# Performance work log

Hardware: AMD Instinct MI355X
Metric: run time of the kernel (lower is better)

The kernel has to match this reference:

```python
import jax, jax.numpy as jnp
import numpy as np

E, N = 400000, 50000
D = 128          # efeat_dim = src_dim = dst_dim = output_dim
H = 512          # hidden_dim
CAT = 3 * D      # concat of [efeat, src, dst]
LN_EPS = 1e-5


def setup_inputs() -> dict:
    key = jax.random.key(0)
    ks = jax.random.split(key, 12)
    scale = 0.02
    return {
        "efeat": jax.random.normal(ks[0], (E, D), jnp.float32),
        "src_feat": jax.random.normal(ks[1], (N, D), jnp.float32),
        "dst_feat": jax.random.normal(ks[2], (N, D), jnp.float32),
        "src_idx": jax.random.randint(ks[3], (E,), 0, N),
        "dst_idx": jax.random.randint(ks[4], (E,), 0, N),
        # MLP params: Linear(CAT,H) -> SiLU -> Linear(H,H) -> SiLU -> Linear(H,D) -> LayerNorm(D)
        "W1": jax.random.normal(ks[5], (CAT, H), jnp.float32) * scale,
        "b1": jnp.zeros((H,), jnp.float32),
        "W2": jax.random.normal(ks[6], (H, H), jnp.float32) * scale,
        "b2": jnp.zeros((H,), jnp.float32),
        "W3": jax.random.normal(ks[7], (H, D), jnp.float32) * scale,
        "b3": jnp.zeros((D,), jnp.float32),
        "gamma": jnp.ones((D,), jnp.float32),
        "beta": jnp.zeros((D,), jnp.float32),
    }


def _layer_norm(y, gamma, beta):
    mu = jnp.mean(y, axis=-1, keepdims=True)
    var = jnp.mean(jnp.square(y - mu), axis=-1, keepdims=True)
    return (y - mu) * jax.lax.rsqrt(var + LN_EPS) * gamma + beta


def reference(efeat, src_feat, dst_feat, src_idx, dst_idx,
              W1, b1, W2, b2, W3, b3, gamma, beta):
    # concat_efeat: per-edge gather of src/dst node feats + concat with edge feats
    cat = jnp.concatenate([efeat, src_feat[src_idx], dst_feat[dst_idx]], axis=1)  # [E, 3D]
    h = jax.nn.silu(cat @ W1 + b1)   # [E, H]
    h = jax.nn.silu(h @ W2 + b2)     # [E, H]
    y = h @ W3 + b3                  # [E, D]
    return _layer_norm(y, gamma, beta)
```

## Files before the change

kernel.cpp:

```cpp
#include <hip/hip_runtime.h>
#include <hip/hip_bf16.h>
#include <cstdint>
#include <cstddef>

typedef __attribute__((ext_vector_type(4))) float f32x4;
typedef __attribute__((ext_vector_type(8))) short s16x8;
typedef __attribute__((ext_vector_type(4))) unsigned int u32x4;

#define E_ 400000
#define D_ 128
#define H_ 512
#define CAT_ 384
#define BM 64
#define NBLK 6250
#define SCRATCH 65536
#define LDS_TOTAL (65536 + 1024)

__device__ __forceinline__ unsigned cvtpk(float lo, float hi) {
  unsigned r;
  asm("v_cvt_pk_bf16_f32 %0, %1, %2" : "=v"(r) : "v"(lo), "v"(hi));
  return r;
}
__device__ __forceinline__ float silu_f(float x) {
  return x * __builtin_amdgcn_rcpf(1.0f + __expf(-x));
}

#define HS(row, byteoff) (smem + (row) * 1024 + ((byteoff) ^ (((row) & 7) << 4)))

__global__ __launch_bounds__(512, 4)
void edge_mlp_fused(const float* __restrict__ efeat,
                    const float* __restrict__ src_feat,
                    const float* __restrict__ dst_feat,
                    const int* __restrict__ src_idx,
                    const int* __restrict__ dst_idx,
                    const unsigned short* __restrict__ P1,
                    const unsigned short* __restrict__ P2,
                    const unsigned short* __restrict__ P3,
                    const float* __restrict__ b1,
                    const float* __restrict__ b2,
                    const float* __restrict__ b3,
                    const float* __restrict__ gamma,
                    const float* __restrict__ beta,
                    float* __restrict__ out) {
  extern __shared__ char smem[];
  const int tid = threadIdx.x;
  const int lane = tid & 63;
  const int wave = tid >> 6;
  const int lr = lane & 15;
  const int kc = lane >> 4;
  const int g4 = kc * 4;
  const size_t e0 = (size_t)blockIdx.x * BM;
  const int rot = ((blockIdx.x >> 8) & 1) << 3;

  const unsigned short* w1base = P1 + (size_t)kc * 4096 + wave * 512 + lr * 8;
  const unsigned short* w2base = P2 + (size_t)kc * 4096 + wave * 512 + lr * 8;

  const int grow = tid >> 3, gq = tid & 7;
  const size_t ee = e0 + grow;

#define LOAD4(dst, base) { const float* s0_ = (base) + gq * 8; \
  dst[0] = *(const f32x4*)s0_;        dst[1] = *(const f32x4*)(s0_ + 4); \
  dst[2] = *(const f32x4*)(s0_ + 64); dst[3] = *(const f32x4*)(s0_ + 68); }

#define STASH(v, scol) { \
  u32x4 r0_, r1_; \
  r0_.x = cvtpk(v[0][0], v[0][1]); r0_.y = cvtpk(v[0][2], v[0][3]); \
  r0_.z = cvtpk(v[1][0], v[1][1]); r0_.w = cvtpk(v[1][2], v[1][3]); \
  r1_.x = cvtpk(v[2][0], v[2][1]); r1_.y = cvtpk(v[2][2], v[2][3]); \
  r1_.z = cvtpk(v[3][0], v[3][1]); r1_.w = cvtpk(v[3][2], v[3][3]); \
  *(u32x4*)HS(grow, ((scol) + gq * 8) * 2) = r0_; \
  *(u32x4*)HS(grow, ((scol) + 64 + gq * 8) * 2) = r1_; }

  {
    f32x4 acc[4][4];
    #pragma unroll
    for (int eg = 0; eg < 4; ++eg)
      #pragma unroll
      for (int j = 0; j < 4; ++j) acc[eg][j] = (f32x4){0.f, 0.f, 0.f, 0.f};

    const float* psrc = src_feat + (size_t)src_idx[ee] * D_;
    const float* pdst = dst_feat + (size_t)dst_idx[ee] * D_;

    f32x4 gx[4], gs[4];
    LOAD4(gx, efeat + ee * D_);
    LOAD4(gs, psrc);
    STASH(gx, 0);

    asm volatile("s_waitcnt lgkmcnt(0)" ::: "memory");
    __builtin_amdgcn_s_barrier();
    asm volatile("" ::: "memory");

    auto g1tier = [&](int P0) {
      const unsigned short* wp = w1base + (size_t)P0 * 16384;
      #pragma unroll 1
      for (int pp = 0; pp < 4; ++pp) {
        s16x8 w[4];
        #pragma unroll
        for (int j = 0; j < 4; ++j)
          w[j] = *(const s16x8*)(wp + j * 128);
        const int p = P0 + pp;
        #pragma unroll
        for (int eg = 0; eg < 4; ++eg) {
          const s16x8 bf = *(const s16x8*)HS(eg * 16 + lr, p * 64 + kc * 16);
          #pragma unroll
          for (int j = 0; j < 4; ++j)
            acc[eg][j] = __builtin_amdgcn_mfma_f32_16x16x32_bf16(w[j], bf, acc[eg][j], 0, 0, 0);
        }
        wp += 16384;
      }
    };

    g1tier(0);
    STASH(gs, 128);
    LOAD4(gx, pdst);
    asm volatile("s_waitcnt lgkmcnt(0)" ::: "memory");
    __builtin_amdgcn_s_barrier();
    asm volatile("" ::: "memory");

    g1tier(4);
    STASH(gx, 256);
    asm volatile("s_waitcnt lgkmcnt(0)" ::: "memory");
    __builtin_amdgcn_s_barrier();
    asm volatile("" ::: "memory");

    g1tier(8);

    __builtin_amdgcn_s_barrier();
    asm volatile("" ::: "memory");

    #pragma unroll
    for (int j = 0; j < 4; ++j) {
      const int col0 = (wave * 4 + j) * 16 + g4;
      const f32x4 bv = *(const f32x4*)(b1 + col0);
      #pragma unroll
      for (int eg = 0; eg < 4; ++eg) {
        uint2 o_;
        o_.x = cvtpk(silu_f(acc[eg][j][0] + bv[0]), silu_f(acc[eg][j][1] + bv[1]));
        o_.y = cvtpk(silu_f(acc[eg][j][2] + bv[2]), silu_f(acc[eg][j][3] + bv[3]));
        *(uint2*)HS(eg * 16 + lr, col0 * 2) = o_;
      }
    }
  }
  asm volatile("s_waitcnt lgkmcnt(0)" ::: "memory");
  __builtin_amdgcn_s_barrier();
  asm volatile("" ::: "memory");

  {
    f32x4 acc[4][4];
    #pragma unroll
    for (int eg = 0; eg < 4; ++eg)
      #pragma unroll
      for (int j = 0; j < 4; ++j) acc[eg][j] = (f32x4){0.f, 0.f, 0.f, 0.f};

    #pragma unroll 2
    for (int pp = 0; pp < 16; ++pp) {
      const int p = (pp + rot) & 15;
      s16x8 w[4];
      #pragma unroll
      for (int j = 0; j < 4; ++j)
        w[j] = *(const s16x8*)(w2base + (size_t)p * 16384 + j * 128);
      #pragma unroll
      for (int eg = 0; eg < 4; ++eg) {
        const s16x8 bf = *(const s16x8*)HS(eg * 16 + lr, p * 64 + kc * 16);
        #pragma unroll
        for (int j = 0; j < 4; ++j)
          acc[eg][j] = __builtin_amdgcn_mfma_f32_16x16x32_bf16(w[j], bf, acc[eg][j], 0, 0, 0);
      }
    }

    __builtin_amdgcn_s_barrier();
    asm volatile("" ::: "memory");

    #pragma unroll
    for (int j = 0; j < 4; ++j) {
      const int col0 = (wave * 4 + j) * 16 + g4;
      const f32x4 bv = *(const f32x4*)(b2 + col0);
      #pragma unroll
      for (int eg = 0; eg < 4; ++eg) {
        uint2 o_;
        o_.x = cvtpk(silu_f(acc[eg][j][0] + bv[0]), silu_f(acc[eg][j][1] + bv[1]));
        o_.y = cvtpk(silu_f(acc[eg][j][2] + bv[2]), silu_f(acc[eg][j][3] + bv[3]));
        *(uint2*)HS(eg * 16 + lr, col0 * 2) = o_;
      }
    }
  }
  asm volatile("s_waitcnt lgkmcnt(0)" ::: "memory");
  __builtin_amdgcn_s_barrier();
  asm volatile("" ::: "memory");

  {
    const int eg3 = wave >> 1;
    const int half = wave & 1;
    const int edge = eg3 * 16 + lr;

    f32x4 acc[4];
    #pragma unroll
    for (int j = 0; j < 4; ++j) acc[j] = (f32x4){0.f, 0.f, 0.f, 0.f};

    const unsigned short* w3b = P3 + (size_t)kc * 1024 + half * 512 + lr * 8;

    #pragma unroll 2
    for (int pp = 0; pp < 16; ++pp) {
      const int p = (pp + rot) & 15;
      s16x8 w[4];
      #pragma unroll
      for (int j = 0; j < 4; ++j)
        w[j] = *(const s16x8*)(w3b + (size_t)p * 4096 + j * 128);
      const s16x8 bf = *(const s16x8*)HS(edge, p * 64 + kc * 16);
      #pragma unroll
      for (int j = 0; j < 4; ++j)
        acc[j] = __builtin_amdgcn_mfma_f32_16x16x32_bf16(w[j], bf, acc[j], 0, 0, 0);
    }

    float sum = 0.f, ss = 0.f;
    #pragma unroll
    for (int j = 0; j < 4; ++j) {
      const f32x4 bv = *(const f32x4*)(b3 + half * 64 + j * 16 + g4);
      #pragma unroll
      for (int r = 0; r < 4; ++r) {
        acc[j][r] += bv[r];
        sum += acc[j][r];
        ss += acc[j][r] * acc[j][r];
      }
    }
    sum += __shfl_xor(sum, 16, 64); ss += __shfl_xor(ss, 16, 64);
    sum += __shfl_xor(sum, 32, 64); ss += __shfl_xor(ss, 32, 64);

    if (lane < 16) {
      float2 pw; pw.x = sum; pw.y = ss;
      *(float2*)(smem + SCRATCH + edge * 16 + half * 8) = pw;
    }
    asm volatile("s_waitcnt lgkmcnt(0)" ::: "memory");
    __builtin_amdgcn_s_barrier();
    asm volatile("" ::: "memory");

    const f32x4 pt = *(const f32x4*)(smem + SCRATCH + edge * 16);
    const float sumT = pt[0] + pt[2];
    const float ssT  = pt[1] + pt[3];
    const float mu = sumT * (1.0f / 128.0f);
    const float var = ssT * (1.0f / 128.0f) - mu * mu;
    const float rstd = rsqrtf(var + 1e-5f);

    float* orow = out + (e0 + edge) * D_ + half * 64;
    #pragma unroll
    for (int j = 0; j < 4; ++j) {
      const f32x4 gv  = *(const f32x4*)(gamma + half * 64 + j * 16 + g4);
      const f32x4 btv = *(const f32x4*)(beta  + half * 64 + j * 16 + g4);
      f32x4 o;
      #pragma unroll
      for (int r = 0; r < 4; ++r)
        o[r] = (acc[j][r] - mu) * rstd * gv[r] + btv[r];
      *(f32x4*)(orow + j * 16 + g4) = o;
    }
  }
#undef LOAD4
#undef STASH
}

__global__ void prep_pack(const float* __restrict__ W, unsigned short* __restrict__ P,
                          int K, int N) {
  const int t = blockIdx.x * blockDim.x + threadIdx.x;
  if (t >= N * (K >> 3)) return;
  const int n = t % N;
  const int k8 = t / N;
  const int k0 = k8 << 3;
  const int p = k0 >> 5, kc = (k0 >> 3) & 3;
  s16x8 w;
  #pragma unroll
  for (int j = 0; j < 8; ++j) {
    union { float f; unsigned u; } t_; t_.f = W[(size_t)(k0 + j) * N + n];
    w[j] = (short)((t_.u + 0x8000u) >> 16);
  }
  *(s16x8*)(P + (size_t)p * N * 32 + (size_t)kc * N * 8 + (size_t)n * 8) = w;
}

extern "C" void kernel_launch(void* const* d_in, const int* in_sizes, int n_in,
                              void* d_out, int out_size, void* d_ws, size_t ws_size,
                              hipStream_t stream) {
  const float* efeat    = (const float*)d_in[0];
  const float* src_feat = (const float*)d_in[1];
  const float* dst_feat = (const float*)d_in[2];
  const int*   src_idx  = (const int*)d_in[3];
  const int*   dst_idx  = (const int*)d_in[4];
  const float* W1 = (const float*)d_in[5];
  const float* b1 = (const float*)d_in[6];
  const float* W2 = (const float*)d_in[7];
  const float* b2 = (const float*)d_in[8];
  const float* W3 = (const float*)d_in[9];
  const float* b3 = (const float*)d_in[10];
  const float* gamma = (const float*)d_in[11];
  const float* beta  = (const float*)d_in[12];

  unsigned short* P1 = (unsigned short*)d_ws;
  unsigned short* P2 = P1 + 196608;
  unsigned short* P3 = P2 + 262144;

  (void)hipFuncSetAttribute((const void*)edge_mlp_fused,
                            hipFuncAttributeMaxDynamicSharedMemorySize, LDS_TOTAL);

  prep_pack<<<(512 * 48 + 255) / 256, 256, 0, stream>>>(W1, P1, CAT_, H_);
  prep_pack<<<(512 * 64 + 255) / 256, 256, 0, stream>>>(W2, P2, H_, H_);
  prep_pack<<<(128 * 64 + 255) / 256, 256, 0, stream>>>(W3, P3, H_, D_);

  edge_mlp_fused<<<NBLK, 512, LDS_TOTAL, stream>>>(
      efeat, src_feat, dst_feat, src_idx, dst_idx,
      P1, P2, P3, b1, b2, b3, gamma, beta, (float*)d_out);
}
```

Before: 531.6 us.

## Double block to 1024 threads, halve per-wave columns, gather inputs upfront

Each block now runs 16 waves over the same 64 edges, so every wave owns 32 hidden columns instead of 64 and half as many accumulators. The staged overlap of gathering src/dst rows with the first GEMM is replaced by one gather of all three feature sources before the first GEMM. The aim is more waves in flight to hide memory latency and lighter register pressure per wave. The cost is that the gather no longer overlaps with compute, and the 1024-thread blocks with about 66KB LDS each may limit how many blocks fit per CU.

After: 543.4 us. 1.02x slower.

```diff
diff --git a/kernel.cpp b/kernel.cpp
--- a/kernel.cpp
+++ b/kernel.cpp
@@ -14,7 +14,7 @@
 #define BM 64
 #define NBLK 6250
 #define SCRATCH 65536
-#define LDS_TOTAL (65536 + 1024)
+#define LDS_TOTAL (65536 + 2048)
 
 __device__ __forceinline__ unsigned cvtpk(float lo, float hi) {
   unsigned r;
@@ -27,7 +27,7 @@
 
 #define HS(row, byteoff) (smem + (row) * 1024 + ((byteoff) ^ (((row) & 7) << 4)))
 
-__global__ __launch_bounds__(512, 4)
+__global__ __launch_bounds__(1024, 8)
 void edge_mlp_fused(const float* __restrict__ efeat,
                     const float* __restrict__ src_feat,
                     const float* __restrict__ dst_feat,
@@ -52,85 +52,59 @@
   const size_t e0 = (size_t)blockIdx.x * BM;
   const int rot = ((blockIdx.x >> 8) & 1) << 3;
 
-  const unsigned short* w1base = P1 + (size_t)kc * 4096 + wave * 512 + lr * 8;
-  const unsigned short* w2base = P2 + (size_t)kc * 4096 + wave * 512 + lr * 8;
-
-  const int grow = tid >> 3, gq = tid & 7;
-  const size_t ee = e0 + grow;
-
-#define LOAD4(dst, base) { const float* s0_ = (base) + gq * 8; \
-  dst[0] = *(const f32x4*)s0_;        dst[1] = *(const f32x4*)(s0_ + 4); \
-  dst[2] = *(const f32x4*)(s0_ + 64); dst[3] = *(const f32x4*)(s0_ + 68); }
-
-#define STASH(v, scol) { \
-  u32x4 r0_, r1_; \
-  r0_.x = cvtpk(v[0][0], v[0][1]); r0_.y = cvtpk(v[0][2], v[0][3]); \
-  r0_.z = cvtpk(v[1][0], v[1][1]); r0_.w = cvtpk(v[1][2], v[1][3]); \
-  r1_.x = cvtpk(v[2][0], v[2][1]); r1_.y = cvtpk(v[2][2], v[2][3]); \
-  r1_.z = cvtpk(v[3][0], v[3][1]); r1_.w = cvtpk(v[3][2], v[3][3]); \
-  *(u32x4*)HS(grow, ((scol) + gq * 8) * 2) = r0_; \
-  *(u32x4*)HS(grow, ((scol) + 64 + gq * 8) * 2) = r1_; }
-
-  {
-    f32x4 acc[4][4];
+  const unsigned short* w1base = P1 + (size_t)kc * 4096 + wave * 256 + lr * 8;
+  const unsigned short* w2base = P2 + (size_t)kc * 4096 + wave * 256 + lr * 8;
+
+  {
+    const int row = tid >> 4, q = tid & 15;
+    const size_t ee = e0 + row;
+    const float* bases[3];
+    bases[0] = efeat + ee * D_;
+    bases[1] = src_feat + (size_t)src_idx[ee] * D_;
+    bases[2] = dst_feat + (size_t)dst_idx[ee] * D_;
+    #pragma unroll
+    for (int s = 0; s < 3; ++s) {
+      const float* sp = bases[s] + q * 8;
+      const f32x4 v0 = *(const f32x4*)sp;
+      const f32x4 v1 = *(const f32x4*)(sp + 4);
+      u32x4 r_;
+      r_.x = cvtpk(v0[0], v0[1]); r_.y = cvtpk(v0[2], v0[3]);
+      r_.z = cvtpk(v1[0], v1[1]); r_.w = cvtpk(v1[2], v1[3]);
+      *(u32x4*)HS(row, (s * 128 + q * 8) * 2) = r_;
+    }
+  }
+  asm volatile("s_waitcnt lgkmcnt(0)" ::: "memory");
+  __builtin_amdgcn_s_barrier();
+  asm volatile("" ::: "memory");
+
+  {
+    f32x4 acc[4][2];
     #pragma unroll
     for (int eg = 0; eg < 4; ++eg)
       #pragma unroll
-      for (int j = 0; j < 4; ++j) acc[eg][j] = (f32x4){0.f, 0.f, 0.f, 0.f};
-
-    const float* psrc = src_feat + (size_t)src_idx[ee] * D_;
-    const float* pdst = dst_feat + (size_t)dst_idx[ee] * D_;
-
-    f32x4 gx[4], gs[4];
-    LOAD4(gx, efeat + ee * D_);
-    LOAD4(gs, psrc);
-    STASH(gx, 0);
-
-    asm volatile("s_waitcnt lgkmcnt(0)" ::: "memory");
+      for (int j = 0; j < 2; ++j) acc[eg][j] = (f32x4){0.f, 0.f, 0.f, 0.f};
+
+    #pragma unroll 2
+    for (int p = 0; p < 12; ++p) {
+      s16x8 w[2];
+      #pragma unroll
+      for (int j = 0; j < 2; ++j)
+        w[j] = *(const s16x8*)(w1base + (size_t)p * 16384 + j * 128);
+      #pragma unroll
+      for (int eg = 0; eg < 4; ++eg) {
+        const s16x8 bf = *(const s16x8*)HS(eg * 16 + lr, p * 64 + kc * 16);
+        #pragma unroll
+        for (int j = 0; j < 2; ++j)
+          acc[eg][j] = __builtin_amdgcn_mfma_f32_16x16x32_bf16(w[j], bf, acc[eg][j], 0, 0, 0);
+      }
+    }
+
     __builtin_amdgcn_s_barrier();
     asm volatile("" ::: "memory");
 
-    auto g1tier = [&](int P0) {
-      const unsigned short* wp = w1base + (size_t)P0 * 16384;
-      #pragma unroll 1
-      for (int pp = 0; pp < 4; ++pp) {
-        s16x8 w[4];
-        #pragma unroll
-        for (int j = 0; j < 4; ++j)
-          w[j] = *(const s16x8*)(wp + j * 128);
-        const int p = P0 + pp;
-        #pragma unroll
-        for (int eg = 0; eg < 4; ++eg) {
-          const s16x8 bf = *(const s16x8*)HS(eg * 16 + lr, p * 64 + kc * 16);
-          #pragma unroll
-          for (int j = 0; j < 4; ++j)
-            acc[eg][j] = __builtin_amdgcn_mfma_f32_16x16x32_bf16(w[j], bf, acc[eg][j], 0, 0, 0);
-        }
-        wp += 16384;
-      }
-    };
-
-    g1tier(0);
-    STASH(gs, 128);
-    LOAD4(gx, pdst);
-    asm volatile("s_waitcnt lgkmcnt(0)" ::: "memory");
-    __builtin_amdgcn_s_barrier();
-    asm volatile("" ::: "memory");
-
-    g1tier(4);
-    STASH(gx, 256);
-    asm volatile("s_waitcnt lgkmcnt(0)" ::: "memory");
-    __builtin_amdgcn_s_barrier();
-    asm volatile("" ::: "memory");
-
-    g1tier(8);
-
-    __builtin_amdgcn_s_barrier();
-    asm volatile("" ::: "memory");
-
-    #pragma unroll
-    for (int j = 0; j < 4; ++j) {
-      const int col0 = (wave * 4 + j) * 16 + g4;
+    #pragma unroll
+    for (int j = 0; j < 2; ++j) {
+      const int col0 = wave * 32 + j * 16 + g4;
       const f32x4 bv = *(const f32x4*)(b1 + col0);
       #pragma unroll
       for (int eg = 0; eg < 4; ++eg) {
@@ -146,24 +120,24 @@
   asm volatile("" ::: "memory");
 
   {
-    f32x4 acc[4][4];
+    f32x4 acc[4][2];
     #pragma unroll
     for (int eg = 0; eg < 4; ++eg)
       #pragma unroll
-      for (int j = 0; j < 4; ++j) acc[eg][j] = (f32x4){0.f, 0.f, 0.f, 0.f};
+      for (int j = 0; j < 2; ++j) acc[eg][j] = (f32x4){0.f, 0.f, 0.f, 0.f};
 
     #pragma unroll 2
     for (int pp = 0; pp < 16; ++pp) {
       const int p = (pp + rot) & 15;
-      s16x8 w[4];
-      #pragma unroll
-      for (int j = 0; j < 4; ++j)
+      s16x8 w[2];
+      #pragma unroll
+      for (int j = 0; j < 2; ++j)
         w[j] = *(const s16x8*)(w2base + (size_t)p * 16384 + j * 128);
       #pragma unroll
       for (int eg = 0; eg < 4; ++eg) {
         const s16x8 bf = *(const s16x8*)HS(eg * 16 + lr, p * 64 + kc * 16);
         #pragma unroll
-        for (int j = 0; j < 4; ++j)
+        for (int j = 0; j < 2; ++j)
           acc[eg][j] = __builtin_amdgcn_mfma_f32_16x16x32_bf16(w[j], bf, acc[eg][j], 0, 0, 0);
       }
     }
@@ -172,8 +146,8 @@
     asm volatile("" ::: "memory");
 
     #pragma unroll
-    for (int j = 0; j < 4; ++j) {
-      const int col0 = (wave * 4 + j) * 16 + g4;
+    for (int j = 0; j < 2; ++j) {
+      const int col0 = wave * 32 + j * 16 + g4;
       const f32x4 bv = *(const f32x4*)(b2 + col0);
       #pragma unroll
       for (int eg = 0; eg < 4; ++eg) {
@@ -189,33 +163,33 @@
   asm volatile("" ::: "memory");
 
   {
-    const int eg3 = wave >> 1;
-    const int half = wave & 1;
+    const int q3 = wave & 3;
+    const int eg3 = wave >> 2;
     const int edge = eg3 * 16 + lr;
 
-    f32x4 acc[4];
-    #pragma unroll
-    for (int j = 0; j < 4; ++j) acc[j] = (f32x4){0.f, 0.f, 0.f, 0.f};
-
-    const unsigned short* w3b = P3 + (size_t)kc * 1024 + half * 512 + lr * 8;
+    f32x4 acc[2];
+    #pragma unroll
+    for (int j = 0; j < 2; ++j) acc[j] = (f32x4){0.f, 0.f, 0.f, 0.f};
+
+    const unsigned short* w3b = P3 + (size_t)kc * 1024 + q3 * 256 + lr * 8;
 
     #pragma unroll 2
     for (int pp = 0; pp < 16; ++pp) {
       const int p = (pp + rot) & 15;
-      s16x8 w[4];
-      #pragma unroll
-      for (int j = 0; j < 4; ++j)
+      s16x8 w[2];
+      #pragma unroll
+      for (int j = 0; j < 2; ++j)
         w[j] = *(const s16x8*)(w3b + (size_t)p * 4096 + j * 128);
       const s16x8 bf = *(const s16x8*)HS(edge, p * 64 + kc * 16);
       #pragma unroll
-      for (int j = 0; j < 4; ++j)
+      for (int j = 0; j < 2; ++j)
         acc[j] = __builtin_amdgcn_mfma_f32_16x16x32_bf16(w[j], bf, acc[j], 0, 0, 0);
     }
 
     float sum = 0.f, ss = 0.f;
     #pragma unroll
-    for (int j = 0; j < 4; ++j) {
-      const f32x4 bv = *(const f32x4*)(b3 + half * 64 + j * 16 + g4);
+    for (int j = 0; j < 2; ++j) {
+      const f32x4 bv = *(const f32x4*)(b3 + q3 * 32 + j * 16 + g4);
       #pragma unroll
       for (int r = 0; r < 4; ++r) {
         acc[j][r] += bv[r];
@@ -228,24 +202,25 @@
 
     if (lane < 16) {
       float2 pw; pw.x = sum; pw.y = ss;
-      *(float2*)(smem + SCRATCH + edge * 16 + half * 8) = pw;
+      *(float2*)(smem + SCRATCH + edge * 32 + q3 * 8) = pw;
     }
     asm volatile("s_waitcnt lgkmcnt(0)" ::: "memory");
     __builtin_amdgcn_s_barrier();
     asm volatile("" ::: "memory");
 
-    const f32x4 pt = *(const f32x4*)(smem + SCRATCH + edge * 16);
-    const float sumT = pt[0] + pt[2];
-    const float ssT  = pt[1] + pt[3];
+    const f32x4 pa = *(const f32x4*)(smem + SCRATCH + edge * 32);
+    const f32x4 pb = *(const f32x4*)(smem + SCRATCH + edge * 32 + 16);
+    const float sumT = pa[0] + pa[2] + pb[0] + pb[2];
+    const float ssT  = pa[1] + pa[3] + pb[1] + pb[3];
     const float mu = sumT * (1.0f / 128.0f);
     const float var = ssT * (1.0f / 128.0f) - mu * mu;
     const float rstd = rsqrtf(var + 1e-5f);
 
-    float* orow = out + (e0 + edge) * D_ + half * 64;
-    #pragma unroll
-    for (int j = 0; j < 4; ++j) {
-      const f32x4 gv  = *(const f32x4*)(gamma + half * 64 + j * 16 + g4);
-      const f32x4 btv = *(const f32x4*)(beta  + half * 64 + j * 16 + g4);
+    float* orow = out + (e0 + edge) * D_ + q3 * 32;
+    #pragma unroll
+    for (int j = 0; j < 2; ++j) {
+      const f32x4 gv  = *(const f32x4*)(gamma + q3 * 32 + j * 16 + g4);
+      const f32x4 btv = *(const f32x4*)(beta  + q3 * 32 + j * 16 + g4);
       f32x4 o;
       #pragma unroll
       for (int r = 0; r < 4; ++r)
@@ -253,8 +228,6 @@
       *(f32x4*)(orow + j * 16 + g4) = o;
     }
   }
-#undef LOAD4
-#undef STASH
 }
 
 __global__ void prep_pack(const float* __restrict__ W, unsigned short* __restrict__ P,
@@ -302,7 +275,7 @@
   prep_pack<<<(512 * 64 + 255) / 256, 256, 0, stream>>>(W2, P2, H_, H_);
   prep_pack<<<(128 * 64 + 255) / 256, 256, 0, stream>>>(W3, P3, H_, D_);
 
-  edge_mlp_fused<<<NBLK, 512, LDS_TOTAL, stream>>>(
+  edge_mlp_fused<<<NBLK, 1024, LDS_TOTAL, stream>>>(
       efeat, src_feat, dst_feat, src_idx, dst_idx,
       P1, P2, P3, b1, b2, b3, gamma, beta, (float*)d_out);
 }
```
